# Kernel optimization log

Hardware: AMD Instinct MI355X
Metric: run time of the kernel (lower is better)

The kernel has to match this reference:

```python
import jax, jax.numpy as jnp
import numpy as np

N_EXPERTS = 8
D_IN = 1024
D_OUT = 1024
BATCH = 4096


def setup_inputs() -> dict:
    key = jax.random.key(0)
    k_x, k_w, k_b, k_a = jax.random.split(key, 4)
    xs = jax.random.normal(k_x, (BATCH, D_IN), dtype=jnp.float32)
    mxs = jnp.arange(BATCH, dtype=jnp.int32)  # opaque per-sample metadata, passed through
    actions = jax.random.randint(k_a, (BATCH,), 0, N_EXPERTS, dtype=jnp.int64)
    # Expert parameters: each submodule is Linear(D_IN -> D_OUT)
    W = jax.random.normal(k_w, (N_EXPERTS, D_OUT, D_IN), dtype=jnp.float32) / np.sqrt(D_IN)
    b = jax.random.normal(k_b, (N_EXPERTS, D_OUT), dtype=jnp.float32) * 0.01
    return {"xs": xs, "mxs": mxs, "actions": actions, "W": W, "b": b}


def reference(xs, mxs, actions, W, b):
    # Original: per-sample python loop y_i = submodule[actions[i]](x_i); cat along batch.
    # Vectorized: compute all experts densely (E small), then select per-sample row.
    y_all = jnp.einsum("bj,eij->bei", xs, W) + b[None, :, :]  # [B, E, D_OUT]
    ys = jnp.take_along_axis(y_all, actions[:, None, None].astype(jnp.int32), axis=1)
    ys = jnp.squeeze(ys, axis=1)  # [B, D_OUT]
    return (ys, mxs, actions)
```

## Files before the change

kernel.cpp:

```cpp
#include <hip/hip_runtime.h>

#define BATCH 4096
#define D_IN 1024
#define D_OUT 1024
#define N_EXPERTS 8

#define TM 64
#define TN 128
#define TK 32
#define MAX_TILES 71

#define WS_PERM    0
#define WS_STARTS  4096
#define WS_TILE_E  4112
#define WS_TILE_M  4200
#define WS_NTILES  4288

typedef __attribute__((ext_vector_type(8))) short short8;
typedef __attribute__((ext_vector_type(4))) float f32x4;

__global__ void group_kernel(const int* __restrict__ actions, int* __restrict__ ws) {
    __shared__ int cnt[N_EXPERTS];
    __shared__ int base[N_EXPERTS];
    const int t = threadIdx.x;
    if (t < N_EXPERTS) cnt[t] = 0;
    __syncthreads();
    for (int i = t; i < BATCH; i += 256) atomicAdd(&cnt[actions[i]], 1);
    __syncthreads();
    if (t == 0) {
        int s = 0, nt = 0;
        for (int e = 0; e < N_EXPERTS; ++e) {
            const int c = cnt[e];
            base[e] = s;
            ws[WS_STARTS + e] = s;
            for (int m0 = 0; m0 < c; m0 += TM) {
                ws[WS_TILE_E + nt] = e;
                ws[WS_TILE_M + nt] = m0;
                ++nt;
            }
            s += c;
            cnt[e] = 0;
        }
        ws[WS_STARTS + N_EXPERTS] = s;
        ws[WS_NTILES] = nt;
    }
    __syncthreads();
    for (int i = t; i < BATCH; i += 256) {
        const int a = actions[i];
        const int pos = base[a] + atomicAdd(&cnt[a], 1);
        ws[WS_PERM + pos] = i;
    }
}

__device__ __forceinline__ void cvt8(const float4 a, const float4 b,
                                     short8& h, short8& l) {
    float f[8] = {a.x, a.y, a.z, a.w, b.x, b.y, b.z, b.w};
#pragma unroll
    for (int i = 0; i < 8; ++i) {
        const unsigned u = __float_as_uint(f[i]);
        h[i] = (short)(u >> 16);
        const float r = f[i] - __uint_as_float(u & 0xffff0000u);
        l[i] = (short)(__float_as_uint(r) >> 16);
    }
}

__global__ __launch_bounds__(256) void moe_gemm(
    const float* __restrict__ xs, const float* __restrict__ W,
    const float* __restrict__ bias, const int* __restrict__ ws,
    float* __restrict__ out)
{
    const int tix = blockIdx.y;
    if (tix >= ws[WS_NTILES]) return;
    const int e   = ws[WS_TILE_E + tix];
    const int m0  = ws[WS_TILE_M + tix];
    const int s0  = ws[WS_STARTS + e];
    const int cnt = ws[WS_STARTS + e + 1] - s0;
    const int n0  = blockIdx.x * TN;

    __shared__ short Ahi[TM * TK];
    __shared__ short Alo[TM * TK];
    __shared__ short Bhi[TN * TK];
    __shared__ short Blo[TN * TK];
    __shared__ int   rows_s[TM];

    const int t = threadIdx.x;
    if (t < TM) {
        const int r = m0 + t;
        rows_s[t] = (r < cnt) ? ws[WS_PERM + s0 + r] : -1;
    }
    __syncthreads();

    const int lane = t & 63;
    const int wave = t >> 6;
    const int wm = (wave & 1) * 32;
    const int wn = (wave >> 1) * 64;

    const float zf = 0.f;
    f32x4 acc[2][4];
#pragma unroll
    for (int mi = 0; mi < 2; ++mi)
#pragma unroll
        for (int nj = 0; nj < 4; ++nj)
            acc[mi][nj] = (f32x4){zf, zf, zf, zf};

    const float* Wb = W + (size_t)e * (D_OUT * (size_t)D_IN) + (size_t)n0 * D_IN;

    const int j  = t & 3;
    const int rr = t >> 2;

    const int arow = rows_s[rr];
    const float* aptr = (arow >= 0) ? (xs + (size_t)arow * D_IN + j * 8) : nullptr;
    const int aoff_st = (rr >> 4) * 512 + (j * 16 + (rr & 15)) * 8;

    for (int k0 = 0; k0 < D_IN; k0 += TK) {
        __syncthreads();
        {
            float4 v0 = make_float4(0.f, 0.f, 0.f, 0.f), v1 = v0;
            if (aptr) {
                v0 = *(const float4*)(aptr + k0);
                v1 = *(const float4*)(aptr + k0 + 4);
            }
            short8 h, l;
            cvt8(v0, v1, h, l);
            *(short8*)&Ahi[aoff_st] = h;
            *(short8*)&Alo[aoff_st] = l;
        }
#pragma unroll
        for (int i = 0; i < 2; ++i) {
            const int n   = i * 64 + rr;
            const int off = (n >> 4) * 512 + (j * 16 + (n & 15)) * 8;
            const float* q = Wb + (size_t)n * D_IN + k0 + j * 8;
            const float4 w0 = *(const float4*)q;
            const float4 w1 = *(const float4*)(q + 4);
            short8 h, l;
            cvt8(w0, w1, h, l);
            *(short8*)&Bhi[off] = h;
            *(short8*)&Blo[off] = l;
        }
        __syncthreads();

        short8 ah[2], al[2], bh[4], bl[4];
#pragma unroll
        for (int i2 = 0; i2 < 2; ++i2) {
            const int aoff = ((wm >> 4) + i2) * 512 + lane * 8;
            ah[i2] = *(const short8*)&Ahi[aoff];
            al[i2] = *(const short8*)&Alo[aoff];
        }
#pragma unroll
        for (int i2 = 0; i2 < 4; ++i2) {
            const int boff = ((wn >> 4) + i2) * 512 + lane * 8;
            bh[i2] = *(const short8*)&Bhi[boff];
            bl[i2] = *(const short8*)&Blo[boff];
        }
#pragma unroll
        for (int mi = 0; mi < 2; ++mi)
#pragma unroll
            for (int nj = 0; nj < 4; ++nj) {
                acc[mi][nj] = __builtin_amdgcn_mfma_f32_16x16x32_bf16(ah[mi], bh[nj], acc[mi][nj], 0, 0, 0);
                acc[mi][nj] = __builtin_amdgcn_mfma_f32_16x16x32_bf16(ah[mi], bl[nj], acc[mi][nj], 0, 0, 0);
                acc[mi][nj] = __builtin_amdgcn_mfma_f32_16x16x32_bf16(al[mi], bh[nj], acc[mi][nj], 0, 0, 0);
            }
    }

    const int cl = lane & 15;
    const int qd = lane >> 4;
    float bv[4];
#pragma unroll
    for (int nj = 0; nj < 4; ++nj)
        bv[nj] = bias[e * D_OUT + n0 + wn + nj * 16 + cl];
#pragma unroll
    for (int mi = 0; mi < 2; ++mi) {
#pragma unroll
        for (int reg = 0; reg < 4; ++reg) {
            const int mloc = wm + mi * 16 + qd * 4 + reg;
            const int r = rows_s[mloc];
            if (r >= 0) {
                float* orow = out + (size_t)r * D_OUT + n0 + wn + cl;
#pragma unroll
                for (int nj = 0; nj < 4; ++nj)
                    orow[nj * 16] = acc[mi][nj][reg] + bv[nj];
            }
        }
    }
}

__global__ void meta_float_kernel(const int* __restrict__ mxs,
                                  const int* __restrict__ actions,
                                  float* __restrict__ out) {
    const int i = blockIdx.x * 256 + threadIdx.x;
    if (i < BATCH) {
        out[BATCH * D_OUT + i] = (float)mxs[i];
        out[BATCH * D_OUT + BATCH + i] = (float)actions[i];
    }
}

__global__ void meta_raw64_kernel(const int* __restrict__ mxs,
                                  const int* __restrict__ actions,
                                  float* __restrict__ out) {
    const int i = blockIdx.x * 256 + threadIdx.x;
    if (i < BATCH) {
        out[BATCH * D_OUT + i] = (float)mxs[i];
        long long* a64 = (long long*)(out + BATCH * D_OUT + BATCH);
        a64[i] = (long long)actions[i];
    }
}

extern "C" void kernel_launch(void* const* d_in, const int* in_sizes, int n_in,
                              void* d_out, int out_size, void* d_ws, size_t ws_size,
                              hipStream_t stream) {
    const float* xs      = (const float*)d_in[0];
    const int*   mxs     = (const int*)d_in[1];
    const int*   actions = (const int*)d_in[2];
    const float* W       = (const float*)d_in[3];
    const float* bias    = (const float*)d_in[4];
    float* out = (float*)d_out;
    int*   ws  = (int*)d_ws;

    group_kernel<<<1, 256, 0, stream>>>(actions, ws);

    dim3 grid(D_OUT / TN, MAX_TILES, 1);
    moe_gemm<<<grid, 256, 0, stream>>>(xs, W, bias, ws, out);

    const int metaOff = BATCH * D_OUT;
    if (out_size >= metaOff + 3 * BATCH) {
        meta_raw64_kernel<<<(BATCH + 255) / 256, 256, 0, stream>>>(mxs, actions, out);
    } else if (out_size >= metaOff + 2 * BATCH) {
        meta_float_kernel<<<(BATCH + 255) / 256, 256, 0, stream>>>(mxs, actions, out);
    }
}
```

Baseline: 158.4 us.

## Pre-split operands to bf16 hi/lo planes and stream W via LDS DMA

Measured after the change: 176.7 us. 1.12x slower.

```diff
diff --git a/kernel.cpp b/kernel.cpp
--- a/kernel.cpp
+++ b/kernel.cpp
@@ -7,7 +7,6 @@
 
 #define TM 64
 #define TN 128
-#define TK 32
 #define MAX_TILES 71
 
 #define WS_PERM    0
@@ -15,6 +14,17 @@
 #define WS_TILE_E  4112
 #define WS_TILE_M  4200
 #define WS_NTILES  4288
+
+#define OFF_WHI  32768
+#define SZ_WPL   (8u*1024u*1024u*2u)
+#define OFF_WLO  (OFF_WHI + SZ_WPL)
+#define OFF_XHI  (OFF_WLO + SZ_WPL)
+#define SZ_XPL   (4u*1024u*1024u*2u)
+#define OFF_XLO  (OFF_XHI + SZ_XPL)
+#define WS_NEED  ((size_t)OFF_XLO + SZ_XPL)
+
+#define W_CHUNKS (N_EXPERTS * 64 * 32 * 64)
+#define X_CHUNKS (BATCH * 128)
 
 typedef __attribute__((ext_vector_type(8))) short short8;
 typedef __attribute__((ext_vector_type(4))) float f32x4;
@@ -64,7 +74,178 @@
     }
 }
 
-__global__ __launch_bounds__(256) void moe_gemm(
+__global__ __launch_bounds__(256) void convert_kernel(
+    const float* __restrict__ xs, const float* __restrict__ W,
+    unsigned short* __restrict__ whi, unsigned short* __restrict__ wlo,
+    unsigned short* __restrict__ xhi, unsigned short* __restrict__ xlo)
+{
+    const int g = blockIdx.x * 256 + threadIdx.x;
+    if (g < W_CHUNKS) {
+        const int lane = g & 63, s = (g >> 6) & 31, nt = (g >> 11) & 63, e = g >> 17;
+        const int n = nt * 16 + (lane & 15);
+        const int k = s * 32 + ((lane >> 4) << 3);
+        const float* src = W + ((size_t)e << 20) + (size_t)n * D_IN + k;
+        const float4 v0 = *(const float4*)src;
+        const float4 v1 = *(const float4*)(src + 4);
+        short8 h, l;
+        cvt8(v0, v1, h, l);
+        ((short8*)whi)[g] = h;
+        ((short8*)wlo)[g] = l;
+    } else {
+        const int gx = g - W_CHUNKS;
+        const float* src = xs + (size_t)gx * 8;
+        const float4 v0 = *(const float4*)src;
+        const float4 v1 = *(const float4*)(src + 4);
+        short8 h, l;
+        cvt8(v0, v1, h, l);
+        ((short8*)xhi)[gx] = h;
+        ((short8*)xlo)[gx] = l;
+    }
+}
+
+__device__ __forceinline__ void load_to_lds16(const unsigned short* g, unsigned short* l) {
+    __builtin_amdgcn_global_load_lds(
+        (const __attribute__((address_space(1))) unsigned int*)(g),
+        (__attribute__((address_space(3))) unsigned int*)(l),
+        16, 0, 0);
+}
+
+__global__ __launch_bounds__(256) void moe_gemm_dma(
+    const unsigned short* __restrict__ xhi, const unsigned short* __restrict__ xlo,
+    const unsigned short* __restrict__ whi, const unsigned short* __restrict__ wlo,
+    const float* __restrict__ bias, const int* __restrict__ ws,
+    float* __restrict__ out)
+{
+    const int bx  = blockIdx.x & 7;
+    const int tix = blockIdx.x >> 3;
+    if (tix >= ws[WS_NTILES]) return;
+    const int e   = ws[WS_TILE_E + tix];
+    const int m0  = ws[WS_TILE_M + tix];
+    const int s0  = ws[WS_STARTS + e];
+    const int cnt = ws[WS_STARTS + e + 1] - s0;
+    const int n0  = bx * TN;
+
+    __shared__ unsigned short Bhi[2][8 * 512];
+    __shared__ unsigned short Blo[2][8 * 512];
+    __shared__ int rows_s[TM];
+
+    const int t = threadIdx.x;
+    if (t < TM) {
+        const int r = m0 + t;
+        rows_s[t] = (r < cnt) ? ws[WS_PERM + s0 + r] : -1;
+    }
+    __syncthreads();
+
+    const int lane = t & 63;
+    const int wave = t >> 6;
+    const int wm = (wave & 1) * 32;
+    const int wn = (wave >> 1) * 64;
+
+    const unsigned short* aSrcHi[2];
+    const unsigned short* aSrcLo[2];
+#pragma unroll
+    for (int mi = 0; mi < 2; ++mi) {
+        int r = rows_s[wm + mi * 16 + (lane & 15)];
+        if (r < 0) r = 0;
+        const size_t off = (size_t)r * D_IN + ((lane >> 4) << 3);
+        aSrcHi[mi] = xhi + off;
+        aSrcLo[mi] = xlo + off;
+    }
+
+    const unsigned short* bsrc[4];
+    const unsigned short* bpl[4];
+    int btile[4];
+#pragma unroll
+    for (int i = 0; i < 4; ++i) {
+        const int c = wave * 4 + i;
+        btile[i] = c >> 1;
+        bpl[i] = (c & 1) ? wlo : whi;
+        bsrc[i] = bpl[i] + (size_t)(e * 64 + bx * 8 + btile[i]) * 16384 + lane * 8;
+    }
+
+    const float zf = 0.f;
+    f32x4 acc[2][4];
+#pragma unroll
+    for (int mi = 0; mi < 2; ++mi)
+#pragma unroll
+        for (int nj = 0; nj < 4; ++nj)
+            acc[mi][nj] = (f32x4){zf, zf, zf, zf};
+
+    short8 ah[2], al[2], ahn[2], aln[2];
+#pragma unroll
+    for (int mi = 0; mi < 2; ++mi) {
+        ah[mi] = *(const short8*)aSrcHi[mi];
+        al[mi] = *(const short8*)aSrcLo[mi];
+        aSrcHi[mi] += 32;
+        aSrcLo[mi] += 32;
+    }
+#pragma unroll
+    for (int i = 0; i < 4; ++i) {
+        load_to_lds16(bsrc[i], ((bpl[i] == whi) ? &Bhi[0][0] : &Blo[0][0]) + btile[i] * 512);
+        bsrc[i] += 512;
+    }
+
+    for (int s = 0; s < 32; ++s) {
+        const int cur = s & 1;
+        __syncthreads();
+        if (s < 31) {
+#pragma unroll
+            for (int mi = 0; mi < 2; ++mi) {
+                ahn[mi] = *(const short8*)aSrcHi[mi];
+                aln[mi] = *(const short8*)aSrcLo[mi];
+                aSrcHi[mi] += 32;
+                aSrcLo[mi] += 32;
+            }
+#pragma unroll
+            for (int i = 0; i < 4; ++i) {
+                load_to_lds16(bsrc[i], ((bpl[i] == whi) ? &Bhi[cur ^ 1][0] : &Blo[cur ^ 1][0]) + btile[i] * 512);
+                bsrc[i] += 512;
+            }
+        }
+        short8 bh[4], bl[4];
+#pragma unroll
+        for (int i2 = 0; i2 < 4; ++i2) {
+            const int boff = ((wn >> 4) + i2) * 512 + lane * 8;
+            bh[i2] = *(const short8*)&Bhi[cur][boff];
+            bl[i2] = *(const short8*)&Blo[cur][boff];
+        }
+#pragma unroll
+        for (int mi = 0; mi < 2; ++mi)
+#pragma unroll
+            for (int nj = 0; nj < 4; ++nj) {
+                acc[mi][nj] = __builtin_amdgcn_mfma_f32_16x16x32_bf16(ah[mi], bh[nj], acc[mi][nj], 0, 0, 0);
+                acc[mi][nj] = __builtin_amdgcn_mfma_f32_16x16x32_bf16(ah[mi], bl[nj], acc[mi][nj], 0, 0, 0);
+                acc[mi][nj] = __builtin_amdgcn_mfma_f32_16x16x32_bf16(al[mi], bh[nj], acc[mi][nj], 0, 0, 0);
+            }
+        if (s < 31) {
+#pragma unroll
+            for (int mi = 0; mi < 2; ++mi) { ah[mi] = ahn[mi]; al[mi] = aln[mi]; }
+        }
+    }
+
+    const int cl = lane & 15;
+    const int qd = lane >> 4;
+    float bv[4];
+#pragma unroll
+    for (int nj = 0; nj < 4; ++nj)
+        bv[nj] = bias[e * D_OUT + n0 + wn + nj * 16 + cl];
+#pragma unroll
+    for (int mi = 0; mi < 2; ++mi) {
+#pragma unroll
+        for (int reg = 0; reg < 4; ++reg) {
+            const int mloc = wm + mi * 16 + qd * 4 + reg;
+            const int r = rows_s[mloc];
+            if (r >= 0) {
+                float* orow = out + (size_t)r * D_OUT + n0 + wn + cl;
+#pragma unroll
+                for (int nj = 0; nj < 4; ++nj)
+                    orow[nj * 16] = acc[mi][nj][reg] + bv[nj];
+            }
+        }
+    }
+}
+
+__global__ __launch_bounds__(256) void moe_gemm_fb(
     const float* __restrict__ xs, const float* __restrict__ W,
     const float* __restrict__ bias, const int* __restrict__ ws,
     float* __restrict__ out)
@@ -77,10 +258,10 @@
     const int cnt = ws[WS_STARTS + e + 1] - s0;
     const int n0  = blockIdx.x * TN;
 
-    __shared__ short Ahi[TM * TK];
-    __shared__ short Alo[TM * TK];
-    __shared__ short Bhi[TN * TK];
-    __shared__ short Blo[TN * TK];
+    __shared__ short Ahi[TM * 32];
+    __shared__ short Alo[TM * 32];
+    __shared__ short Bhi[TN * 32];
+    __shared__ short Blo[TN * 32];
     __shared__ int   rows_s[TM];
 
     const int t = threadIdx.x;
@@ -104,15 +285,13 @@
             acc[mi][nj] = (f32x4){zf, zf, zf, zf};
 
     const float* Wb = W + (size_t)e * (D_OUT * (size_t)D_IN) + (size_t)n0 * D_IN;
-
     const int j  = t & 3;
     const int rr = t >> 2;
-
     const int arow = rows_s[rr];
     const float* aptr = (arow >= 0) ? (xs + (size_t)arow * D_IN + j * 8) : nullptr;
     const int aoff_st = (rr >> 4) * 512 + (j * 16 + (rr & 15)) * 8;
 
-    for (int k0 = 0; k0 < D_IN; k0 += TK) {
+    for (int k0 = 0; k0 < D_IN; k0 += 32) {
         __syncthreads();
         {
             float4 v0 = make_float4(0.f, 0.f, 0.f, 0.f), v1 = v0;
@@ -218,8 +397,17 @@
 
     group_kernel<<<1, 256, 0, stream>>>(actions, ws);
 
-    dim3 grid(D_OUT / TN, MAX_TILES, 1);
-    moe_gemm<<<grid, 256, 0, stream>>>(xs, W, bias, ws, out);
+    if (ws_size >= WS_NEED) {
+        unsigned short* whi = (unsigned short*)((char*)d_ws + OFF_WHI);
+        unsigned short* wlo = (unsigned short*)((char*)d_ws + OFF_WLO);
+        unsigned short* xhi = (unsigned short*)((char*)d_ws + OFF_XHI);
+        unsigned short* xlo = (unsigned short*)((char*)d_ws + OFF_XLO);
+        convert_kernel<<<(W_CHUNKS + X_CHUNKS) / 256, 256, 0, stream>>>(xs, W, whi, wlo, xhi, xlo);
+        moe_gemm_dma<<<8 * MAX_TILES, 256, 0, stream>>>(xhi, xlo, whi, wlo, bias, ws, out);
+    } else {
+        dim3 grid(D_OUT / TN, MAX_TILES, 1);
+        moe_gemm_fb<<<grid, 256, 0, stream>>>(xs, W, bias, ws, out);
+    }
 
     const int metaOff = BATCH * D_OUT;
     if (out_size >= metaOff + 3 * BATCH) {
```

## Retile MoE GEMM to 64x64x64, flatten grid with swizzle, fold metadata into grouping

Applied to the files above, without the earlier changes.

After: 190.1 us. 20.1% more time.

```diff
diff --git a/kernel.cpp b/kernel.cpp
--- a/kernel.cpp
+++ b/kernel.cpp
@@ -6,8 +6,8 @@
 #define N_EXPERTS 8
 
 #define TM 64
-#define TN 128
-#define TK 32
+#define TN 64
+#define TK 64
 #define MAX_TILES 71
 
 #define WS_PERM    0
@@ -19,13 +19,27 @@
 typedef __attribute__((ext_vector_type(8))) short short8;
 typedef __attribute__((ext_vector_type(4))) float f32x4;
 
-__global__ void group_kernel(const int* __restrict__ actions, int* __restrict__ ws) {
+__global__ void group_kernel(const int* __restrict__ actions,
+                             const int* __restrict__ mxs,
+                             int* __restrict__ ws,
+                             float* __restrict__ out, int meta_mode) {
     __shared__ int cnt[N_EXPERTS];
     __shared__ int base[N_EXPERTS];
     const int t = threadIdx.x;
     if (t < N_EXPERTS) cnt[t] = 0;
     __syncthreads();
-    for (int i = t; i < BATCH; i += 256) atomicAdd(&cnt[actions[i]], 1);
+    const int M = BATCH * D_OUT;
+    for (int i = t; i < BATCH; i += 256) {
+        const int a = actions[i];
+        atomicAdd(&cnt[a], 1);
+        if (meta_mode == 1) {
+            out[M + i] = (float)mxs[i];
+            out[M + BATCH + i] = (float)a;
+        } else if (meta_mode == 2) {
+            out[M + i] = (float)mxs[i];
+            ((long long*)(out + M + BATCH))[i] = (long long)a;
+        }
+    }
     __syncthreads();
     if (t == 0) {
         int s = 0, nt = 0;
@@ -64,18 +78,19 @@
     }
 }
 
-__global__ __launch_bounds__(256) void moe_gemm(
+__global__ __launch_bounds__(256, 4) void moe_gemm(
     const float* __restrict__ xs, const float* __restrict__ W,
     const float* __restrict__ bias, const int* __restrict__ ws,
     float* __restrict__ out)
 {
-    const int tix = blockIdx.y;
+    const int nx  = ((blockIdx.x & 7) << 1) | ((blockIdx.x >> 3) & 1);
+    const int tix = blockIdx.x >> 4;
     if (tix >= ws[WS_NTILES]) return;
     const int e   = ws[WS_TILE_E + tix];
     const int m0  = ws[WS_TILE_M + tix];
     const int s0  = ws[WS_STARTS + e];
     const int cnt = ws[WS_STARTS + e + 1] - s0;
-    const int n0  = blockIdx.x * TN;
+    const int n0  = nx * TN;
 
     __shared__ short Ahi[TM * TK];
     __shared__ short Alo[TM * TK];
@@ -93,80 +108,70 @@
     const int lane = t & 63;
     const int wave = t >> 6;
     const int wm = (wave & 1) * 32;
-    const int wn = (wave >> 1) * 64;
+    const int wn = (wave >> 1) * 32;
 
     const float zf = 0.f;
-    f32x4 acc[2][4];
+    f32x4 acc[2][2];
 #pragma unroll
     for (int mi = 0; mi < 2; ++mi)
 #pragma unroll
-        for (int nj = 0; nj < 4; ++nj)
+        for (int nj = 0; nj < 2; ++nj)
             acc[mi][nj] = (f32x4){zf, zf, zf, zf};
 
-    const float* Wb = W + (size_t)e * (D_OUT * (size_t)D_IN) + (size_t)n0 * D_IN;
-
-    const int j  = t & 3;
-    const int rr = t >> 2;
-
-    const int arow = rows_s[rr];
-    const float* aptr = (arow >= 0) ? (xs + (size_t)arow * D_IN + j * 8) : nullptr;
-    const int aoff_st = (rr >> 4) * 512 + (j * 16 + (rr & 15)) * 8;
+    const int li = t & 15;
+    const int kq = (t >> 4) & 3;
+    const int row_l = (t >> 6) * 16 + li;
+    const int arow = rows_s[row_l];
+    const float* ap = xs + (size_t)((arow < 0) ? 0 : arow) * D_IN + kq * 8;
+    const float* bp = W + ((size_t)e << 20) + (size_t)(n0 + row_l) * D_IN + kq * 8;
+    const int st = t * 8;
 
     for (int k0 = 0; k0 < D_IN; k0 += TK) {
         __syncthreads();
-        {
-            float4 v0 = make_float4(0.f, 0.f, 0.f, 0.f), v1 = v0;
-            if (aptr) {
-                v0 = *(const float4*)(aptr + k0);
-                v1 = *(const float4*)(aptr + k0 + 4);
+#pragma unroll
+        for (int kt = 0; kt < 2; ++kt) {
+            const float4 a0 = *(const float4*)(ap + k0 + kt * 32);
+            const float4 a1 = *(const float4*)(ap + k0 + kt * 32 + 4);
+            short8 h, l;
+            cvt8(a0, a1, h, l);
+            *(short8*)&Ahi[kt * 2048 + st] = h;
+            *(short8*)&Alo[kt * 2048 + st] = l;
+            const float4 b0 = *(const float4*)(bp + k0 + kt * 32);
+            const float4 b1 = *(const float4*)(bp + k0 + kt * 32 + 4);
+            cvt8(b0, b1, h, l);
+            *(short8*)&Bhi[kt * 2048 + st] = h;
+            *(short8*)&Blo[kt * 2048 + st] = l;
+        }
+        __syncthreads();
+
+#pragma unroll
+        for (int kt = 0; kt < 2; ++kt) {
+            short8 ah[2], al[2], bh[2], bl[2];
+#pragma unroll
+            for (int i2 = 0; i2 < 2; ++i2) {
+                const int aoff = kt * 2048 + ((wm >> 4) + i2) * 512 + lane * 8;
+                ah[i2] = *(const short8*)&Ahi[aoff];
+                al[i2] = *(const short8*)&Alo[aoff];
+                const int boff = kt * 2048 + ((wn >> 4) + i2) * 512 + lane * 8;
+                bh[i2] = *(const short8*)&Bhi[boff];
+                bl[i2] = *(const short8*)&Blo[boff];
             }
-            short8 h, l;
-            cvt8(v0, v1, h, l);
-            *(short8*)&Ahi[aoff_st] = h;
-            *(short8*)&Alo[aoff_st] = l;
-        }
-#pragma unroll
-        for (int i = 0; i < 2; ++i) {
-            const int n   = i * 64 + rr;
-            const int off = (n >> 4) * 512 + (j * 16 + (n & 15)) * 8;
-            const float* q = Wb + (size_t)n * D_IN + k0 + j * 8;
-            const float4 w0 = *(const float4*)q;
-            const float4 w1 = *(const float4*)(q + 4);
-            short8 h, l;
-            cvt8(w0, w1, h, l);
-            *(short8*)&Bhi[off] = h;
-            *(short8*)&Blo[off] = l;
-        }
-        __syncthreads();
-
-        short8 ah[2], al[2], bh[4], bl[4];
-#pragma unroll
-        for (int i2 = 0; i2 < 2; ++i2) {
-            const int aoff = ((wm >> 4) + i2) * 512 + lane * 8;
-            ah[i2] = *(const short8*)&Ahi[aoff];
-            al[i2] = *(const short8*)&Alo[aoff];
-        }
-#pragma unroll
-        for (int i2 = 0; i2 < 4; ++i2) {
-            const int boff = ((wn >> 4) + i2) * 512 + lane * 8;
-            bh[i2] = *(const short8*)&Bhi[boff];
-            bl[i2] = *(const short8*)&Blo[boff];
-        }
-#pragma unroll
-        for (int mi = 0; mi < 2; ++mi)
-#pragma unroll
-            for (int nj = 0; nj < 4; ++nj) {
-                acc[mi][nj] = __builtin_amdgcn_mfma_f32_16x16x32_bf16(ah[mi], bh[nj], acc[mi][nj], 0, 0, 0);
-                acc[mi][nj] = __builtin_amdgcn_mfma_f32_16x16x32_bf16(ah[mi], bl[nj], acc[mi][nj], 0, 0, 0);
-                acc[mi][nj] = __builtin_amdgcn_mfma_f32_16x16x32_bf16(al[mi], bh[nj], acc[mi][nj], 0, 0, 0);
-            }
+#pragma unroll
+            for (int mi = 0; mi < 2; ++mi)
+#pragma unroll
+                for (int nj = 0; nj < 2; ++nj) {
+                    acc[mi][nj] = __builtin_amdgcn_mfma_f32_16x16x32_bf16(ah[mi], bh[nj], acc[mi][nj], 0, 0, 0);
+                    acc[mi][nj] = __builtin_amdgcn_mfma_f32_16x16x32_bf16(ah[mi], bl[nj], acc[mi][nj], 0, 0, 0);
+                    acc[mi][nj] = __builtin_amdgcn_mfma_f32_16x16x32_bf16(al[mi], bh[nj], acc[mi][nj], 0, 0, 0);
+                }
+        }
     }
 
     const int cl = lane & 15;
     const int qd = lane >> 4;
-    float bv[4];
-#pragma unroll
-    for (int nj = 0; nj < 4; ++nj)
+    float bv[2];
+#pragma unroll
+    for (int nj = 0; nj < 2; ++nj)
         bv[nj] = bias[e * D_OUT + n0 + wn + nj * 16 + cl];
 #pragma unroll
     for (int mi = 0; mi < 2; ++mi) {
@@ -177,31 +182,10 @@
             if (r >= 0) {
                 float* orow = out + (size_t)r * D_OUT + n0 + wn + cl;
 #pragma unroll
-                for (int nj = 0; nj < 4; ++nj)
+                for (int nj = 0; nj < 2; ++nj)
                     orow[nj * 16] = acc[mi][nj][reg] + bv[nj];
             }
         }
-    }
-}
-
-__global__ void meta_float_kernel(const int* __restrict__ mxs,
-                                  const int* __restrict__ actions,
-                                  float* __restrict__ out) {
-    const int i = blockIdx.x * 256 + threadIdx.x;
-    if (i < BATCH) {
-        out[BATCH * D_OUT + i] = (float)mxs[i];
-        out[BATCH * D_OUT + BATCH + i] = (float)actions[i];
-    }
-}
-
-__global__ void meta_raw64_kernel(const int* __restrict__ mxs,
-                                  const int* __restrict__ actions,
-                                  float* __restrict__ out) {
-    const int i = blockIdx.x * 256 + threadIdx.x;
-    if (i < BATCH) {
-        out[BATCH * D_OUT + i] = (float)mxs[i];
-        long long* a64 = (long long*)(out + BATCH * D_OUT + BATCH);
-        a64[i] = (long long)actions[i];
     }
 }
 
@@ -216,15 +200,12 @@
     float* out = (float*)d_out;
     int*   ws  = (int*)d_ws;
 
-    group_kernel<<<1, 256, 0, stream>>>(actions, ws);
-
-    dim3 grid(D_OUT / TN, MAX_TILES, 1);
-    moe_gemm<<<grid, 256, 0, stream>>>(xs, W, bias, ws, out);
-
     const int metaOff = BATCH * D_OUT;
-    if (out_size >= metaOff + 3 * BATCH) {
-        meta_raw64_kernel<<<(BATCH + 255) / 256, 256, 0, stream>>>(mxs, actions, out);
-    } else if (out_size >= metaOff + 2 * BATCH) {
-        meta_float_kernel<<<(BATCH + 255) / 256, 256, 0, stream>>>(mxs, actions, out);
-    }
-}
+    int meta_mode = 0;
+    if (out_size >= metaOff + 3 * BATCH) meta_mode = 2;
+    else if (out_size >= metaOff + 2 * BATCH) meta_mode = 1;
+
+    group_kernel<<<1, 256, 0, stream>>>(actions, mxs, ws, out, meta_mode);
+
+    moe_gemm<<<16 * MAX_TILES, 256, 0, stream>>>(xs, W, bias, ws, out);
+}
```

## Fuse metadata copy into grouping kernel and replace atomics with prefix-sum scan

Applied to the files above, without the earlier changes.

After: 160.0 us. About the same (+1.0%).

```diff
diff --git a/kernel.cpp b/kernel.cpp
--- a/kernel.cpp
+++ b/kernel.cpp
@@ -19,19 +19,57 @@
 typedef __attribute__((ext_vector_type(8))) short short8;
 typedef __attribute__((ext_vector_type(4))) float f32x4;
 
-__global__ void group_kernel(const int* __restrict__ actions, int* __restrict__ ws) {
-    __shared__ int cnt[N_EXPERTS];
-    __shared__ int base[N_EXPERTS];
+__global__ __launch_bounds__(256) void group_kernel(
+    const int* __restrict__ actions, const int* __restrict__ mxs,
+    int* __restrict__ ws, float* __restrict__ out, int meta_mode) {
+    __shared__ int h[256][N_EXPERTS];
+    __shared__ int starts_s[N_EXPERTS];
+
     const int t = threadIdx.x;
-    if (t < N_EXPERTS) cnt[t] = 0;
+    const int i0 = t * 16;
+    int a_loc[16];
+    int lc[N_EXPERTS];
+#pragma unroll
+    for (int e = 0; e < N_EXPERTS; ++e) lc[e] = 0;
+
+    const int M = BATCH * D_OUT;
+#pragma unroll
+    for (int i = 0; i < 16; ++i) {
+        const int a = actions[i0 + i];
+        a_loc[i] = a;
+        ++lc[a];
+        if (meta_mode == 1) {
+            out[M + i0 + i] = (float)mxs[i0 + i];
+            out[M + BATCH + i0 + i] = (float)a;
+        } else if (meta_mode == 2) {
+            out[M + i0 + i] = (float)mxs[i0 + i];
+            ((long long*)(out + M + BATCH))[i0 + i] = (long long)a;
+        }
+    }
+#pragma unroll
+    for (int e = 0; e < N_EXPERTS; ++e) h[t][e] = lc[e];
     __syncthreads();
-    for (int i = t; i < BATCH; i += 256) atomicAdd(&cnt[actions[i]], 1);
-    __syncthreads();
+
+    for (int d = 1; d < 256; d <<= 1) {
+        int v[N_EXPERTS];
+        const bool act = (t >= d);
+        if (act) {
+#pragma unroll
+            for (int e = 0; e < N_EXPERTS; ++e) v[e] = h[t - d][e];
+        }
+        __syncthreads();
+        if (act) {
+#pragma unroll
+            for (int e = 0; e < N_EXPERTS; ++e) h[t][e] += v[e];
+        }
+        __syncthreads();
+    }
+
     if (t == 0) {
         int s = 0, nt = 0;
         for (int e = 0; e < N_EXPERTS; ++e) {
-            const int c = cnt[e];
-            base[e] = s;
+            const int c = h[255][e];
+            starts_s[e] = s;
             ws[WS_STARTS + e] = s;
             for (int m0 = 0; m0 < c; m0 += TM) {
                 ws[WS_TILE_E + nt] = e;
@@ -39,16 +77,21 @@
                 ++nt;
             }
             s += c;
-            cnt[e] = 0;
         }
         ws[WS_STARTS + N_EXPERTS] = s;
         ws[WS_NTILES] = nt;
     }
     __syncthreads();
-    for (int i = t; i < BATCH; i += 256) {
-        const int a = actions[i];
-        const int pos = base[a] + atomicAdd(&cnt[a], 1);
-        ws[WS_PERM + pos] = i;
+
+    int off[N_EXPERTS];
+#pragma unroll
+    for (int e = 0; e < N_EXPERTS; ++e)
+        off[e] = starts_s[e] + h[t][e] - lc[e];
+#pragma unroll
+    for (int i = 0; i < 16; ++i) {
+        const int a = a_loc[i];
+        ws[WS_PERM + off[a]] = i0 + i;
+        ++off[a];
     }
 }
 
@@ -104,10 +147,8 @@
             acc[mi][nj] = (f32x4){zf, zf, zf, zf};
 
     const float* Wb = W + (size_t)e * (D_OUT * (size_t)D_IN) + (size_t)n0 * D_IN;
-
     const int j  = t & 3;
     const int rr = t >> 2;
-
     const int arow = rows_s[rr];
     const float* aptr = (arow >= 0) ? (xs + (size_t)arow * D_IN + j * 8) : nullptr;
     const int aoff_st = (rr >> 4) * 512 + (j * 16 + (rr & 15)) * 8;
@@ -184,27 +225,6 @@
     }
 }
 
-__global__ void meta_float_kernel(const int* __restrict__ mxs,
-                                  const int* __restrict__ actions,
-                                  float* __restrict__ out) {
-    const int i = blockIdx.x * 256 + threadIdx.x;
-    if (i < BATCH) {
-        out[BATCH * D_OUT + i] = (float)mxs[i];
-        out[BATCH * D_OUT + BATCH + i] = (float)actions[i];
-    }
-}
-
-__global__ void meta_raw64_kernel(const int* __restrict__ mxs,
-                                  const int* __restrict__ actions,
-                                  float* __restrict__ out) {
-    const int i = blockIdx.x * 256 + threadIdx.x;
-    if (i < BATCH) {
-        out[BATCH * D_OUT + i] = (float)mxs[i];
-        long long* a64 = (long long*)(out + BATCH * D_OUT + BATCH);
-        a64[i] = (long long)actions[i];
-    }
-}
-
 extern "C" void kernel_launch(void* const* d_in, const int* in_sizes, int n_in,
                               void* d_out, int out_size, void* d_ws, size_t ws_size,
                               hipStream_t stream) {
@@ -216,15 +236,13 @@
     float* out = (float*)d_out;
     int*   ws  = (int*)d_ws;
 
-    group_kernel<<<1, 256, 0, stream>>>(actions, ws);
+    const int metaOff = BATCH * D_OUT;
+    int meta_mode = 0;
+    if (out_size >= metaOff + 3 * BATCH) meta_mode = 2;
+    else if (out_size >= metaOff + 2 * BATCH) meta_mode = 1;
+
+    group_kernel<<<1, 256, 0, stream>>>(actions, mxs, ws, out, meta_mode);
 
     dim3 grid(D_OUT / TN, MAX_TILES, 1);
     moe_gemm<<<grid, 256, 0, stream>>>(xs, W, bias, ws, out);
-
-    const int metaOff = BATCH * D_OUT;
-    if (out_size >= metaOff + 3 * BATCH) {
-        meta_raw64_kernel<<<(BATCH + 255) / 256, 256, 0, stream>>>(mxs, actions, out);
-    } else if (out_size >= metaOff + 2 * BATCH) {
-        meta_float_kernel<<<(BATCH + 255) / 256, 256, 0, stream>>>(mxs, actions, out);
-    }
-}
+}
```
